# Optimization experiments

Hardware: AMD Instinct MI355X
Metric: run time of the kernel (lower is better)

## Reference

```python
import jax, jax.numpy as jnp
import numpy as np
from jax import lax

L = 50      # observation_len
P = 30      # pred_len
N = 2048    # num nearby obstacles
EMB = 64    # embed_size
NH = 128    # node_hidden_size
EH = 256    # edge_hidden_size
AD = 64     # attention_dim
CNN = 2048  # resnet50 fc.in_features


def setup_inputs() -> dict:
    key = jax.random.key(0)
    ks = jax.random.split(key, 20)
    def rn(k, shape, s=1.0):
        return jax.random.normal(k, shape, jnp.float32) * s
    w = 0.05
    return {
        "img_embedding": rn(ks[0], (1, CNN)),
        "target_obs_pos": rn(ks[1], (1, L, 2)),
        "target_obs_pos_rel": rn(ks[2], (1, L, 2)),
        "nearby_obs_pos": rn(ks[3], (1, N, L, 2)),
        "nearby_obs_pos_rel": rn(ks[4], (1, N, L, 2)),
        "nearby_obs_hist_sizes": jax.random.randint(ks[5], (1, N, 1), 0, L + 1),
        "target_obs_hist_size": L,
        "target_h0": rn(ks[6], (NH,), w),
        "target_c0": rn(ks[7], (NH,), w),
        "W_temb": rn(ks[8], (2, EMB), w), "b_temb": jnp.zeros((EMB,), jnp.float32),
        "Wih_t": rn(ks[9], (EMB, 4 * NH), w), "Whh_t": rn(ks[10], (NH, 4 * NH), w),
        "bih_t": jnp.zeros((4 * NH,), jnp.float32), "bhh_t": jnp.zeros((4 * NH,), jnp.float32),
        "W_tatt": rn(ks[11], (2, AD), w), "b_tatt": jnp.zeros((AD,), jnp.float32),
        "nearby_h0": rn(ks[12], (EH,), w),
        "nearby_c0": rn(ks[13], (EH,), w),
        "W_nemb": rn(ks[14], (2, EMB), w), "b_nemb": jnp.zeros((EMB,), jnp.float32),
        "Wih_n": rn(ks[15], (EMB, 4 * EH), w), "Whh_n": rn(ks[16], (EH, 4 * EH), w),
        "bih_n": jnp.zeros((4 * EH,), jnp.float32), "bhh_n": jnp.zeros((4 * EH,), jnp.float32),
        "W_natt": rn(ks[17], (2, AD), w), "b_natt": jnp.zeros((AD,), jnp.float32),
        "W_pred": rn(ks[18], (NH + CNN + EH, 2), w), "b_pred": jnp.zeros((2,), jnp.float32),
    }


def _lstm_cell(x, h, c, Wih, Whh, bih, bhh, H):
    # PyTorch LSTM gate order: i, f, g, o
    g = x @ Wih + h @ Whh + bih + bhh
    i = jax.nn.sigmoid(g[..., :H])
    f = jax.nn.sigmoid(g[..., H:2 * H])
    gg = jnp.tanh(g[..., 2 * H:3 * H])
    o = jax.nn.sigmoid(g[..., 3 * H:])
    c2 = f * c + i * gg
    return o * jnp.tanh(c2), c2


def _forward(img_embedding, target_obs_pos, target_obs_pos_rel, nearby_obs_pos,
             nearby_obs_pos_rel, target_h0, target_c0, W_temb, b_temb,
             Wih_t, Whh_t, bih_t, bhh_t, W_tatt, b_tatt,
             nearby_h0, nearby_c0, W_nemb, b_nemb,
             Wih_n, Whh_n, bih_n, bhh_n, W_natt, b_natt,
             W_pred, b_pred, nearby_obs_hist_sizes, target_obs_hist_size):
    nhist = nearby_obs_hist_sizes.reshape(N)
    inv_sqrt_d = 1.0 / jnp.sqrt(jnp.float32(AD))

    def attention(trel, tpos, npos, nh, nmask, Ht_prev):
        # scores scaled by curr_N / sqrt(attention_dim), softmax over masked nearby.
        # max-subtracted softmax is mathematically identical to the original exp/sum.
        currN = jnp.sum(nmask.astype(jnp.float32))
        an = (tpos - npos) @ W_natt + b_natt          # [N, AD]
        at = trel @ W_tatt + b_tatt                   # [AD]
        scores = (an @ at) * currN * inv_sqrt_d       # [N]
        w = jax.nn.softmax(jnp.where(nmask, scores, -1e30))
        return jnp.where(currN >= 1.0, w @ nh, Ht_prev)

    def obs_step(carry, x):
        th, tc, nh, nc, Ht = carry
        t, tpos, trel, npos, nrel = x
        tmask = target_obs_hist_size > (L - t)
        nmask = nhist > (L - t)
        th2, tc2 = _lstm_cell(trel @ W_temb + b_temb, th, tc, Wih_t, Whh_t, bih_t, bhh_t, NH)
        th = jnp.where(tmask, th2, th)
        tc = jnp.where(tmask, tc2, tc)
        nh2, nc2 = _lstm_cell(nrel @ W_nemb + b_nemb, nh, nc, Wih_n, Whh_n, bih_n, bhh_n, EH)
        m = nmask[:, None]
        nh = jnp.where(m, nh2, nh)
        nc = jnp.where(m, nc2, nc)
        Ht = attention(trel, tpos, npos, nh, nmask, Ht)
        return (th, tc, nh, nc, Ht), None

    np_tm = jnp.swapaxes(nearby_obs_pos[0], 0, 1)      # [L, N, 2] time-major
    nr_tm = jnp.swapaxes(nearby_obs_pos_rel[0], 0, 1)
    xs = (jnp.arange(1, L), target_obs_pos[0, 1:], target_obs_pos_rel[0, 1:],
          np_tm[1:], nr_tm[1:])
    init = (target_h0, target_c0,
            jnp.broadcast_to(nearby_h0, (N, EH)),
            jnp.broadcast_to(nearby_c0, (N, EH)),
            nearby_h0)
    (th, tc, nh, nc, Ht), _ = lax.scan(obs_step, init, xs)

    # During prediction the original reuses nearby pos/rel from the last obs step.
    npos_last = nearby_obs_pos[0, :, L - 1, :]
    nrel_last = nearby_obs_pos_rel[0, :, L - 1, :]
    xn_last = nrel_last @ W_nemb + b_nemb
    all_mask = jnp.ones((N,), bool)

    def pred_step(carry, _):
        th, tc, nh, nc, Ht, pos = carry
        pred = jnp.concatenate([th, img_embedding[0], Ht]) @ W_pred + b_pred  # [2]
        pos = pos + pred
        th, tc = _lstm_cell(pred @ W_temb + b_temb, th, tc, Wih_t, Whh_t, bih_t, bhh_t, NH)
        nh, nc = _lstm_cell(xn_last, nh, nc, Wih_n, Whh_n, bih_n, bhh_n, EH)
        Ht = attention(pred, pos, npos_last, nh, all_mask, Ht)
        return (th, tc, nh, nc, Ht, pos), pred

    carry0 = (th, tc, nh, nc, Ht, target_obs_pos[0, L - 1])
    _, preds = lax.scan(pred_step, carry0, None, length=P)
    return preds[None]                                 # [1, P, 2]


def reference(img_embedding, target_obs_pos, target_obs_pos_rel, nearby_obs_pos,
              nearby_obs_pos_rel, nearby_obs_hist_sizes, target_obs_hist_size,
              target_h0, target_c0, W_temb, b_temb, Wih_t, Whh_t, bih_t, bhh_t,
              W_tatt, b_tatt, nearby_h0, nearby_c0, W_nemb, b_nemb,
              Wih_n, Whh_n, bih_n, bhh_n, W_natt, b_natt, W_pred, b_pred):
    return _forward(img_embedding, target_obs_pos, target_obs_pos_rel, nearby_obs_pos,
                    nearby_obs_pos_rel, target_h0, target_c0, W_temb, b_temb,
                    Wih_t, Whh_t, bih_t, bhh_t, W_tatt, b_tatt,
                    nearby_h0, nearby_c0, W_nemb, b_nemb,
                    Wih_n, Whh_n, bih_n, bhh_n, W_natt, b_natt,
                    W_pred, b_pred, nearby_obs_hist_sizes, target_obs_hist_size)
```

## Files before the change

### kernel.cpp

```cpp
#include <hip/hip_runtime.h>
#include <hip/hip_bf16.h>
#include <cstdint>

#define LH   50
#define PP   30
#define NAG  2048
#define NHID 128
#define EHID 256
#define ADIM 64
#define CNND 2048

typedef __attribute__((ext_vector_type(8))) short bf16x8;
typedef __attribute__((ext_vector_type(4))) float f32x4;

enum : int {
  WS_WT  = 0,
  WS_WHT = 131072,
  WS_WFN = 163840,
  WS_BFN = 165888,
  WS_WFT = 166912,
  WS_BFT = 167936,
  WS_TH  = 168448,
  WS_TC  = 168576,
  WS_W49 = 168704,
  WS_CN  = 170752,
  WS_Z   = 170756,
  WS_END = 293636
};

__device__ __forceinline__ float sigf(float x){ return 1.0f/(1.0f + __expf(-x)); }
__device__ __forceinline__ float tanhfast(float x){
  x = fminf(15.0f, fmaxf(-15.0f, x));
  float e = __expf(2.0f*x);
  return (e - 1.0f)/(e + 1.0f);
}
__device__ __forceinline__ float bfs(short s){
  return __uint_as_float(((unsigned)(unsigned short)s) << 16);
}
__device__ __forceinline__ void gld16(const void* g, void* l){
  __builtin_amdgcn_global_load_lds(
      (const __attribute__((address_space(1))) unsigned int*)g,
      (__attribute__((address_space(3))) unsigned int*)l, 16, 0, 0);
}

__global__ void k_prep(const float* __restrict__ Whhn, const float* __restrict__ Whht,
                       const float* __restrict__ Wnemb, const float* __restrict__ bnemb,
                       const float* __restrict__ Wihn,  const float* __restrict__ bihn,
                       const float* __restrict__ bhhn,
                       const float* __restrict__ Wtemb, const float* __restrict__ btemb,
                       const float* __restrict__ Wiht,  const float* __restrict__ biht,
                       const float* __restrict__ bhht,
                       float* __restrict__ ws)
{
  const int b = blockIdx.x, tid = threadIdx.x;
  if (b < 256){
    __shared__ float t[32][33];
    __hip_bfloat16* WT = (__hip_bfloat16*)(ws + WS_WT);
    const int tx = tid & 31, ty = tid >> 5;
    const int j0 = (b & 31) << 5;
    const int e0 = (b >> 5) << 5;
    #pragma unroll
    for (int r = 0; r < 4; ++r)
      t[ty + 8*r][tx] = Whhn[(e0 + ty + 8*r)*1024 + j0 + tx];
    __syncthreads();
    const int c = e0 >> 5;
    #pragma unroll
    for (int r = 0; r < 4; ++r)
      WT[c*32768 + (j0 + ty + 8*r)*32 + tx] = __float2bfloat16(t[tx][ty + 8*r]);
  } else {
    for (int j = tid; j < 1024; j += 256){
      float a0=0.f, a1=0.f, ab=0.f;
      for (int k=0;k<64;k++){
        const float w = Wihn[k*1024 + j];
        a0 += Wnemb[k]*w; a1 += Wnemb[64+k]*w; ab += bnemb[k]*w;
      }
      ws[WS_WFN + j]        = a0;
      ws[WS_WFN + 1024 + j] = a1;
      ws[WS_BFN + j]        = ab + bihn[j] + bhhn[j];
    }
    for (int j = tid; j < 512; j += 256){
      float a0=0.f, a1=0.f, ab=0.f;
      for (int k=0;k<64;k++){
        const float w = Wiht[k*512 + j];
        a0 += Wtemb[k]*w; a1 += Wtemb[64+k]*w; ab += btemb[k]*w;
      }
      ws[WS_WFT + j]       = a0;
      ws[WS_WFT + 512 + j] = a1;
      ws[WS_BFT + j]       = ab + biht[j] + bhht[j];
    }
    __hip_bfloat16* WTt = (__hip_bfloat16*)(ws + WS_WHT);
    for (int j = tid; j < 512; j += 256)
      for (int k = 0; k < 128; ++k)
        WTt[j*128 + k] = __float2bfloat16(Whht[k*512 + j]);
  }
}

__global__ __launch_bounds__(512, 2) void k_phaseA(
    const float* __restrict__ nh0, const float* __restrict__ nc0,
    const float* __restrict__ nrel, const int* __restrict__ nhist,
    const float* __restrict__ Wpred,
    const float* __restrict__ trel, const int* __restrict__ thsp,
    const float* __restrict__ Whht, const float* __restrict__ th0,
    const float* __restrict__ tc0,
    const float* __restrict__ tpos, const float* __restrict__ npos,
    const float* __restrict__ Wtatt, const float* __restrict__ btatt,
    const float* __restrict__ Wnatt, const float* __restrict__ bnatt,
    float* __restrict__ ws)
{
  extern __shared__ char smem_raw[];
  const int b = blockIdx.x, tid = threadIdx.x;
  const int wv = tid >> 6, lane = tid & 63;
  const int lhi = lane >> 4, llo = lane & 15;

  if (b < 128){
    short* wbuf = (short*)smem_raw;
    short* Hl   = (short*)(smem_raw + 131072);
    float* relS = (float*)(smem_raw + 139520);
    float* vS   = (float*)(smem_raw + 145920);
    const int n0 = b << 4;

    for (int i = tid; i < 1600; i += 512){
      const int a = i / 100, r = i % 100;
      relS[a*100 + r] = nrel[(n0 + a)*100 + r];
    }
    if (tid < 256){
      vS[2*tid]   = Wpred[2*(NHID + CNND + tid)];
      vS[2*tid+1] = Wpred[2*(NHID + CNND + tid) + 1];
    }
    for (int i = tid; i < 4096; i += 512){
      const int a = i >> 8, e = i & 255;
      ((__hip_bfloat16*)Hl)[a*264 + e] = __float2bfloat16(nh0[e]);
    }

    float wf0[4][2], wf1[4][2], wb[4][2];
    #pragma unroll
    for (int g = 0; g < 4; ++g)
      #pragma unroll
      for (int t = 0; t < 2; ++t){
        const int j = g*256 + (wv<<5) + t*16 + llo;
        wf0[g][t] = ws[WS_WFN + j];
        wf1[g][t] = ws[WS_WFN + 1024 + j];
        wb [g][t] = ws[WS_BFN + j];
      }
    float C[4][2], ho[4][2];
    #pragma unroll
    for (int r = 0; r < 4; ++r)
      #pragma unroll
      for (int t = 0; t < 2; ++t){
        const int eo = (wv<<5) + t*16 + llo;
        C[r][t]  = nc0[eo];
        ho[r][t] = nh0[eo];
      }
    int nh4[4];
    #pragma unroll
    for (int r = 0; r < 4; ++r) nh4[r] = nhist[n0 + lhi*4 + r];

    const char* wgbase = (const char*)(ws + WS_WT);
    __syncthreads();

    {
      const char* gsrc = wgbase + wv*8192 + lane*16;
      char* ldst = (char*)wbuf + wv*8192;
      #pragma unroll
      for (int i = 0; i < 8; ++i) gld16(gsrc + i*1024, ldst + i*1024);
    }
    __syncthreads();
    int cur = 0;

    for (int st = 1; st <= 78; ++st){
      const int thr  = (st <= 49) ? (50 - st) : -1;
      const int tsel = (st <= 49) ? st : 49;

      bf16x8 af[8];
      const short* hrow = Hl + llo*264 + lhi*8;
      #pragma unroll
      for (int c = 0; c < 8; ++c) af[c] = *(const bf16x8*)(hrow + c*32);

      f32x4 acc[4][2];
      #pragma unroll
      for (int g = 0; g < 4; ++g)
        #pragma unroll
        for (int t = 0; t < 2; ++t) acc[g][t] = (f32x4){0.f,0.f,0.f,0.f};

      #pragma unroll
      for (int c = 0; c < 8; ++c){
        {
          const int nc = (c + 1) & 7;
          const char* gsrc = wgbase + nc*65536 + wv*8192 + lane*16;
          char* ldst = (char*)wbuf + (cur^1)*65536 + wv*8192;
          #pragma unroll
          for (int i = 0; i < 8; ++i) gld16(gsrc + i*1024, ldst + i*1024);
        }
        const short* bbase = wbuf + cur*32768;
        #pragma unroll
        for (int g = 0; g < 4; ++g)
          #pragma unroll
          for (int t = 0; t < 2; ++t){
            const int j = g*256 + (wv<<5) + t*16 + llo;
            const bf16x8 bf = *(const bf16x8*)(bbase + j*32 + lhi*8);
            acc[g][t] = __builtin_amdgcn_mfma_f32_16x16x32_bf16(af[c], bf, acc[g][t], 0,0,0);
          }
        __syncthreads();
        cur ^= 1;
      }

      #pragma unroll
      for (int r = 0; r < 4; ++r){
        const float r0 = relS[(lhi*4 + r)*100 + 2*tsel];
        const float r1 = relS[(lhi*4 + r)*100 + 2*tsel + 1];
        const bool mk = nh4[r] > thr;
        #pragma unroll
        for (int t = 0; t < 2; ++t){
          const float gi = acc[0][t][r] + r0*wf0[0][t] + r1*wf1[0][t] + wb[0][t];
          const float gf = acc[1][t][r] + r0*wf0[1][t] + r1*wf1[1][t] + wb[1][t];
          const float gg = acc[2][t][r] + r0*wf0[2][t] + r1*wf1[2][t] + wb[2][t];
          const float go = acc[3][t][r] + r0*wf0[3][t] + r1*wf1[3][t] + wb[3][t];
          const float c2 = sigf(gf)*C[r][t] + sigf(gi)*tanhfast(gg);
          const float h2 = sigf(go)*tanhfast(c2);
          if (mk){ C[r][t] = c2; ho[r][t] = h2; }
        }
      }
      #pragma unroll
      for (int r = 0; r < 4; ++r)
        #pragma unroll
        for (int t = 0; t < 2; ++t)
          ((__hip_bfloat16*)Hl)[(lhi*4 + r)*264 + (wv<<5) + t*16 + llo] =
              __float2bfloat16(ho[r][t]);
      __syncthreads();

      if (st >= 49){
        const int s = st - 49;
        const int a = wv*2 + (lane >> 5);
        const int sub = lane & 31;
        float z0 = 0.f, z1 = 0.f;
        const short* hp = Hl + a*264 + sub*8;
        #pragma unroll
        for (int i = 0; i < 8; ++i){
          const float h = bfs(hp[i]);
          z0 += h*vS[2*(sub*8 + i)];
          z1 += h*vS[2*(sub*8 + i) + 1];
        }
        #pragma unroll
        for (int o = 16; o > 0; o >>= 1){
          z0 += __shfl_down(z0, o, 32);
          z1 += __shfl_down(z1, o, 32);
        }
        if (sub == 0){
          ws[WS_Z + (s*NAG + n0 + a)*2]     = z0;
          ws[WS_Z + (s*NAG + n0 + a)*2 + 1] = z1;
        }
      }
    }
  }
  else if (b == 128){
    float* hT = (float*)smem_raw;
    float* cT = hT + 128;
    float* gT = cT + 128;
    if (tid < 128){ hT[tid] = th0[tid]; cT[tid] = tc0[tid]; }
    __syncthreads();
    const int ths = thsp[0];
    for (int t = 1; t < 50; ++t){
      const float x0 = trel[2*t], x1 = trel[2*t+1];
      float acc = x0*ws[WS_WFT + tid] + x1*ws[WS_WFT + 512 + tid] + ws[WS_BFT + tid];
      for (int k = 0; k < 128; ++k) acc += hT[k]*Whht[k*512 + tid];
      gT[tid] = acc;
      __syncthreads();
      if (tid < 128 && ths > 50 - t){
        const float ig = sigf(gT[tid]),          fg = sigf(gT[128 + tid]);
        const float gg = tanhfast(gT[256 + tid]), og = sigf(gT[384 + tid]);
        const float c2 = fg*cT[tid] + ig*gg;
        cT[tid] = c2; hT[tid] = og*tanhfast(c2);
      }
      __syncthreads();
    }
    if (tid < 128){ ws[WS_TH + tid] = hT[tid]; ws[WS_TC + tid] = cT[tid]; }
  }
  else {
    float* at  = (float*)smem_raw;
    float* red = at + 64;
    float* uv  = red + 512;
    const int t = LH - 1;
    const float tr0 = trel[2*t], tr1 = trel[2*t+1];
    const float tp0 = tpos[2*t], tp1 = tpos[2*t+1];
    if (tid < ADIM) at[tid] = tr0*Wtatt[tid] + tr1*Wtatt[ADIM+tid] + btatt[tid];
    int cnt = 0;
    #pragma unroll
    for (int i = 0; i < 4; ++i) cnt += (nhist[tid + 512*i] > (LH - t)) ? 1 : 0;
    red[tid] = (float)cnt;
    __syncthreads();
    if (tid == 0){
      float u0=0.f,u1=0.f,v=0.f;
      for (int k=0;k<ADIM;k++){ u0 += Wnatt[k]*at[k]; u1 += Wnatt[ADIM+k]*at[k]; v += bnatt[k]*at[k]; }
      uv[0]=u0; uv[1]=u1; uv[2]=v;
    }
    for (int s = 256; s > 0; s >>= 1){ if (tid < s) red[tid] += red[tid+s]; __syncthreads(); }
    const float currN = red[0];
    __syncthreads();
    const float u0 = uv[0], u1 = uv[1], v = uv[2];
    const float scale = currN * 0.125f;
    float sc[4]; float smax = -3.0e38f;
    #pragma unroll
    for (int i = 0; i < 4; ++i){
      const int n = tid + 512*i;
      const float p0 = npos[n*100 + 2*t], p1 = npos[n*100 + 2*t + 1];
      float s = scale * ((tp0-p0)*u0 + (tp1-p1)*u1 + v);
      s = (nhist[n] > (LH - t)) ? s : -1.0e30f;
      sc[i] = s; smax = fmaxf(smax, s);
    }
    red[tid] = smax; __syncthreads();
    for (int s = 256; s > 0; s >>= 1){ if (tid<s) red[tid] = fmaxf(red[tid], red[tid+s]); __syncthreads(); }
    smax = red[0]; __syncthreads();
    float ssum = 0.f;
    #pragma unroll
    for (int i = 0; i < 4; ++i){ sc[i] = __expf(sc[i]-smax); ssum += sc[i]; }
    red[tid] = ssum; __syncthreads();
    for (int s = 256; s > 0; s >>= 1){ if (tid<s) red[tid] += red[tid+s]; __syncthreads(); }
    const float inv = 1.0f / red[0];
    #pragma unroll
    for (int i = 0; i < 4; ++i) ws[WS_W49 + tid + 512*i] = sc[i]*inv;
    if (tid == 0) ws[WS_CN] = currN;
  }
}

template<int K>
__device__ __forceinline__ void bredN(const float* v, volatile float* scratch,
                                      volatile float* outv, int tid){
  const int lane = tid & 63, wv = tid >> 6;
  #pragma unroll
  for (int k = 0; k < K; ++k){
    float x = v[k];
    #pragma unroll
    for (int o = 32; o > 0; o >>= 1) x += __shfl_down(x, o, 64);
    if (lane == 0) scratch[k*8 + wv] = x;
  }
  __syncthreads();
  if (tid == 0){
    #pragma unroll
    for (int k = 0; k < K; ++k){
      float s = 0.f;
      for (int i = 0; i < 8; ++i) s += scratch[k*8 + i];
      outv[k] = s;
    }
  }
  __syncthreads();
}

__device__ __forceinline__ float bredMax1(float x, volatile float* scratch,
                                          volatile float* outv, int tid){
  const int lane = tid & 63, wv = tid >> 6;
  #pragma unroll
  for (int o = 32; o > 0; o >>= 1) x = fmaxf(x, __shfl_down(x, o, 64));
  if (lane == 0) scratch[wv] = x;
  __syncthreads();
  if (tid == 0){
    float s = -3.0e38f;
    for (int i = 0; i < 8; ++i) s = fmaxf(s, scratch[i]);
    outv[0] = s;
  }
  __syncthreads();
  return outv[0];
}

__global__ __launch_bounds__(512, 1) void k_phaseB(
    const float* __restrict__ img, const float* __restrict__ tpos,
    const float* __restrict__ npos, const float* __restrict__ nh0,
    const float* __restrict__ Wpred, const float* __restrict__ bpred,
    const float* __restrict__ Wtatt, const float* __restrict__ btatt,
    const float* __restrict__ Wnatt, const float* __restrict__ bnatt,
    float* __restrict__ ws, float* __restrict__ out)
{
  __shared__ float p0s[NAG], p1s[NAG];
  __shared__ float th[128], tc[128], gl[512], at[64];
// ... 110 lines not shown
      float uu1 = Wnatt[ADIM + lane]*at[lane];
      float vv  = bnatt[lane]*at[lane];
      #pragma unroll
      for (int o = 32; o > 0; o >>= 1){
        uu0 += __shfl_down(uu0, o, 64);
        uu1 += __shfl_down(uu1, o, 64);
        vv  += __shfl_down(vv,  o, 64);
      }
      if (lane == 0){
        bc[4] = uu0; bc[5] = uu1;
        bc[6] = pos0*uu0 + pos1*uu1 + vv;
      }
    }
    __syncthreads();
    u0 = bc[4]; u1 = bc[5]; A = bc[6];
  }
}

extern "C" void kernel_launch(void* const* d_in, const int* in_sizes, int n_in,
                              void* d_out, int out_size, void* d_ws, size_t ws_size,
                              hipStream_t stream) {
  const float* img   = (const float*)d_in[0];
  const float* tpos  = (const float*)d_in[1];
  const float* trel  = (const float*)d_in[2];
  const float* npos  = (const float*)d_in[3];
  const float* nrel  = (const float*)d_in[4];
  const int*   nhist = (const int*)d_in[5];
  const int*   ths   = (const int*)d_in[6];
  const float* th0   = (const float*)d_in[7];
  const float* tc0   = (const float*)d_in[8];
  const float* Wtemb = (const float*)d_in[9];
  const float* btemb = (const float*)d_in[10];
  const float* Wiht  = (const float*)d_in[11];
  const float* Whht  = (const float*)d_in[12];
  const float* biht  = (const float*)d_in[13];
  const float* bhht  = (const float*)d_in[14];
  const float* Wtatt = (const float*)d_in[15];
  const float* btatt = (const float*)d_in[16];
  const float* nh0   = (const float*)d_in[17];
  const float* nc0   = (const float*)d_in[18];
  const float* Wnemb = (const float*)d_in[19];
  const float* bnemb = (const float*)d_in[20];
  const float* Wihn  = (const float*)d_in[21];
  const float* Whhn  = (const float*)d_in[22];
  const float* bihn  = (const float*)d_in[23];
  const float* bhhn  = (const float*)d_in[24];
  const float* Wnatt = (const float*)d_in[25];
  const float* bnatt = (const float*)d_in[26];
  const float* Wpred = (const float*)d_in[27];
  const float* bpred = (const float*)d_in[28];
  float* ws  = (float*)d_ws;
  float* out = (float*)d_out;

  k_prep<<<257, 256, 0, stream>>>(Whhn, Whht, Wnemb, bnemb, Wihn, bihn, bhhn,
                                  Wtemb, btemb, Wiht, biht, bhht, ws);
  k_phaseA<<<130, 512, 147968, stream>>>(nh0, nc0, nrel, nhist, Wpred,
                                         trel, ths, Whht, th0, tc0,
                                         tpos, npos, Wtatt, btatt, Wnatt, bnatt, ws);
  k_phaseB<<<1, 512, 0, stream>>>(img, tpos, npos, nh0, Wpred, bpred,
                                  Wtatt, btatt, Wnatt, bnatt, ws, out);
}
```

Measured before the change: 890.3 us.

## Keep half of recurrent LSTM weights in registers, stream rest with swizzled LDS

The first half of the K dimension of the nearby-agent recurrent weight matrix now lives in per-wave registers for the whole recurrence. Only the second half is streamed from global memory through a double-buffered LDS ring, using a new XOR-swizzled layout built in the prep kernel. Manual waitcnt/s_barrier fences replace __syncthreads, and the H row stride is padded to reduce bank conflicts. This halves per-step weight traffic into LDS at the cost of much higher register pressure and more fragile hand-written synchronisation.

```diff
diff --git a/kernel.cpp b/kernel.cpp
--- a/kernel.cpp
+++ b/kernel.cpp
@@ -15,6 +15,7 @@
 
 enum : int {
   WS_WT  = 0,
+  WS_WZ  = 65536,
   WS_WHT = 131072,
   WS_WFN = 163840,
   WS_BFN = 165888,
@@ -28,6 +29,8 @@
   WS_END = 293636
 };
 
+#define HLROW 280
+
 __device__ __forceinline__ float sigf(float x){ return 1.0f/(1.0f + __expf(-x)); }
 __device__ __forceinline__ float tanhfast(float x){
   x = fminf(15.0f, fmaxf(-15.0f, x));
@@ -53,7 +56,7 @@
                        float* __restrict__ ws)
 {
   const int b = blockIdx.x, tid = threadIdx.x;
-  if (b < 256){
+  if (b < 128){
     __shared__ float t[32][33];
     __hip_bfloat16* WT = (__hip_bfloat16*)(ws + WS_WT);
     const int tx = tid & 31, ty = tid >> 5;
@@ -67,6 +70,19 @@
     #pragma unroll
     for (int r = 0; r < 4; ++r)
       WT[c*32768 + (j0 + ty + 8*r)*32 + tx] = __float2bfloat16(t[tx][ty + 8*r]);
+  } else if (b < 192){
+    __hip_bfloat16* WZ = (__hip_bfloat16*)(ws + WS_WZ);
+    const int bb = b - 128;
+    const int c  = bb >> 4;
+    const int r0 = (bb & 15) << 5;
+    const int r  = r0 + (tid >> 3);
+    const int p  = tid & 7;
+    const int ls = p ^ (r & 7);
+    const int j  = ((ls >> 2) << 9) + r;
+    const int kb = (4 + c)*32 + (ls & 3)*8;
+    #pragma unroll
+    for (int i = 0; i < 8; ++i)
+      WZ[((c*512 + r)*8 + p)*8 + i] = __float2bfloat16(Whhn[(kb + i)*1024 + j]);
   } else {
     for (int j = tid; j < 1024; j += 256){
       float a0=0.f, a1=0.f, ab=0.f;
@@ -115,10 +131,33 @@
   if (b < 128){
     short* wbuf = (short*)smem_raw;
     short* Hl   = (short*)(smem_raw + 131072);
-    float* relS = (float*)(smem_raw + 139520);
-    float* vS   = (float*)(smem_raw + 145920);
+    float* relS = (float*)(smem_raw + 131072 + 16*HLROW*2);
+    float* vS   = relS + 1600;
     const int n0 = b << 4;
 
+    {
+      const char* wz = (const char*)(ws + WS_WZ);
+      #pragma unroll
+      for (int bufc = 0; bufc < 2; ++bufc){
+        const char* gsrc = wz + bufc*65536 + wv*8192 + lane*16;
+        char* ldst = smem_raw + bufc*65536 + wv*8192;
+        #pragma unroll
+        for (int i = 0; i < 8; ++i) gld16(gsrc + i*1024, ldst + i*1024);
+      }
+    }
+    bf16x8 wreg[4][2][4];
+    {
+      const short* wt = (const short*)(ws + WS_WT);
+      #pragma unroll
+      for (int g = 0; g < 4; ++g)
+        #pragma unroll
+        for (int t = 0; t < 2; ++t){
+          const int j = g*256 + (wv<<5) + t*16 + llo;
+          #pragma unroll
+          for (int ks = 0; ks < 4; ++ks)
+            wreg[g][t][ks] = *(const bf16x8*)(wt + ks*32768 + j*32 + lhi*8);
+        }
+    }
     for (int i = tid; i < 1600; i += 512){
       const int a = i / 100, r = i % 100;
       relS[a*100 + r] = nrel[(n0 + a)*100 + r];
@@ -129,9 +168,8 @@
     }
     for (int i = tid; i < 4096; i += 512){
       const int a = i >> 8, e = i & 255;
-      ((__hip_bfloat16*)Hl)[a*264 + e] = __float2bfloat16(nh0[e]);
-    }
-
+      ((__hip_bfloat16*)Hl)[a*HLROW + e] = __float2bfloat16(nh0[e]);
+    }
     float wf0[4][2], wf1[4][2], wb[4][2];
     #pragma unroll
     for (int g = 0; g < 4; ++g)
@@ -155,27 +193,12 @@
     #pragma unroll
     for (int r = 0; r < 4; ++r) nh4[r] = nhist[n0 + lhi*4 + r];
 
-    const char* wgbase = (const char*)(ws + WS_WT);
-    __syncthreads();
-
-    {
-      const char* gsrc = wgbase + wv*8192 + lane*16;
-      char* ldst = (char*)wbuf + wv*8192;
-      #pragma unroll
-      for (int i = 0; i < 8; ++i) gld16(gsrc + i*1024, ldst + i*1024);
-    }
-    __syncthreads();
-    int cur = 0;
+    __syncthreads();
 
     for (int st = 1; st <= 78; ++st){
       const int thr  = (st <= 49) ? (50 - st) : -1;
       const int tsel = (st <= 49) ? st : 49;
 
-      bf16x8 af[8];
-      const short* hrow = Hl + llo*264 + lhi*8;
-      #pragma unroll
-      for (int c = 0; c < 8; ++c) af[c] = *(const bf16x8*)(hrow + c*32);
-
       f32x4 acc[4][2];
       #pragma unroll
       for (int g = 0; g < 4; ++g)
@@ -183,25 +206,44 @@
         for (int t = 0; t < 2; ++t) acc[g][t] = (f32x4){0.f,0.f,0.f,0.f};
 
       #pragma unroll
-      for (int c = 0; c < 8; ++c){
-        {
-          const int nc = (c + 1) & 7;
-          const char* gsrc = wgbase + nc*65536 + wv*8192 + lane*16;
-          char* ldst = (char*)wbuf + (cur^1)*65536 + wv*8192;
+      for (int ks = 0; ks < 4; ++ks){
+        const bf16x8 afr = *(const bf16x8*)(Hl + llo*HLROW + ks*32 + lhi*8);
+        #pragma unroll
+        for (int g = 0; g < 4; ++g)
           #pragma unroll
-          for (int i = 0; i < 8; ++i) gld16(gsrc + i*1024, ldst + i*1024);
-        }
-        const short* bbase = wbuf + cur*32768;
+          for (int t = 0; t < 2; ++t)
+            acc[g][t] = __builtin_amdgcn_mfma_f32_16x16x32_bf16(afr, wreg[g][t][ks], acc[g][t], 0,0,0);
+      }
+
+      #pragma unroll
+      for (int i = 0; i < 4; ++i){
+        const bf16x8 afs = *(const bf16x8*)(Hl + llo*HLROW + (4+i)*32 + lhi*8);
+        asm volatile("s_waitcnt vmcnt(8)" ::: "memory");
+        __builtin_amdgcn_sched_barrier(0);
+        __builtin_amdgcn_s_barrier();
+        __builtin_amdgcn_sched_barrier(0);
+        const short* bb = wbuf + (i & 1)*32768;
         #pragma unroll
         for (int g = 0; g < 4; ++g)
           #pragma unroll
           for (int t = 0; t < 2; ++t){
-            const int j = g*256 + (wv<<5) + t*16 + llo;
-            const bf16x8 bf = *(const bf16x8*)(bbase + j*32 + lhi*8);
-            acc[g][t] = __builtin_amdgcn_mfma_f32_16x16x32_bf16(af[c], bf, acc[g][t], 0,0,0);
+            const int r  = ((g & 1) << 8) + (wv << 5) + t*16 + llo;
+            const int ls = ((g >> 1) << 2) + lhi;
+            const int p  = ls ^ (r & 7);
+            const bf16x8 bfv = *(const bf16x8*)(bb + r*64 + p*8);
+            acc[g][t] = __builtin_amdgcn_mfma_f32_16x16x32_bf16(afs, bfv, acc[g][t], 0,0,0);
           }
-        __syncthreads();
-        cur ^= 1;
+        asm volatile("s_waitcnt lgkmcnt(0)" ::: "memory");
+        __builtin_amdgcn_sched_barrier(0);
+        __builtin_amdgcn_s_barrier();
+        __builtin_amdgcn_sched_barrier(0);
+        {
+          const int nc = (i + 2) & 3;
+          const char* gsrc = (const char*)(ws + WS_WZ) + nc*65536 + wv*8192 + lane*16;
+          char* ldst = smem_raw + (i & 1)*65536 + wv*8192;
+          #pragma unroll
+          for (int q = 0; q < 8; ++q) gld16(gsrc + q*1024, ldst + q*1024);
+        }
       }
 
       #pragma unroll
@@ -224,16 +266,19 @@
       for (int r = 0; r < 4; ++r)
         #pragma unroll
         for (int t = 0; t < 2; ++t)
-          ((__hip_bfloat16*)Hl)[(lhi*4 + r)*264 + (wv<<5) + t*16 + llo] =
+          ((__hip_bfloat16*)Hl)[(lhi*4 + r)*HLROW + (wv<<5) + t*16 + llo] =
               __float2bfloat16(ho[r][t]);
-      __syncthreads();
+      asm volatile("s_waitcnt lgkmcnt(0)" ::: "memory");
+      __builtin_amdgcn_sched_barrier(0);
+      __builtin_amdgcn_s_barrier();
+      __builtin_amdgcn_sched_barrier(0);
 
       if (st >= 49){
         const int s = st - 49;
         const int a = wv*2 + (lane >> 5);
         const int sub = lane & 31;
         float z0 = 0.f, z1 = 0.f;
-        const short* hp = Hl + a*264 + sub*8;
+        const short* hp = Hl + a*HLROW + sub*8;
         #pragma unroll
         for (int i = 0; i < 8; ++i){
           const float h = bfs(hp[i]);
@@ -534,11 +579,13 @@
   float* ws  = (float*)d_ws;
   float* out = (float*)d_out;
 
-  k_prep<<<257, 256, 0, stream>>>(Whhn, Whht, Wnemb, bnemb, Wihn, bihn, bhhn,
+  const int ldsA = 131072 + 16*HLROW*2 + 1600*4 + 512*4;
+
+  k_prep<<<193, 256, 0, stream>>>(Whhn, Whht, Wnemb, bnemb, Wihn, bihn, bhhn,
                                   Wtemb, btemb, Wiht, biht, bhht, ws);
-  k_phaseA<<<130, 512, 147968, stream>>>(nh0, nc0, nrel, nhist, Wpred,
-                                         trel, ths, Whht, th0, tc0,
-                                         tpos, npos, Wtatt, btatt, Wnatt, bnatt, ws);
+  k_phaseA<<<130, 512, ldsA, stream>>>(nh0, nc0, nrel, nhist, Wpred,
+                                       trel, ths, Whht, th0, tc0,
+                                       tpos, npos, Wtatt, btatt, Wnatt, bnatt, ws);
   k_phaseB<<<1, 512, 0, stream>>>(img, tpos, npos, nh0, Wpred, bpred,
                                   Wtatt, btatt, Wnatt, bnatt, ws, out);
 }
```

Result: slower. 937.6 us (+5.3%).

## Keep recurrent LSTM weights resident in registers and LDS instead of restreaming

Applied to the files above, without the earlier changes.

The nearby-agent LSTM kernel previously streamed the full bf16 Whh matrix from global memory into double-buffered LDS on every one of the 78 steps, with a barrier per chunk. Now each block loads the weights once: 6 of 8 K-chunks live in VGPRs per wave and the other 2 sit in LDS. The hidden state is double-buffered in LDS so only one barrier per step is needed. This removes repeated global weight traffic and the per-chunk syncs, at the cost of very high register pressure, with launch bounds relaxed to 1 block per CU.

```diff
diff --git a/kernel.cpp b/kernel.cpp
--- a/kernel.cpp
+++ b/kernel.cpp
@@ -28,6 +28,8 @@
   WS_END = 293636
 };
 
+#define HLH 4224
+
 __device__ __forceinline__ float sigf(float x){ return 1.0f/(1.0f + __expf(-x)); }
 __device__ __forceinline__ float tanhfast(float x){
   x = fminf(15.0f, fmaxf(-15.0f, x));
@@ -36,11 +38,6 @@
 }
 __device__ __forceinline__ float bfs(short s){
   return __uint_as_float(((unsigned)(unsigned short)s) << 16);
-}
-__device__ __forceinline__ void gld16(const void* g, void* l){
-  __builtin_amdgcn_global_load_lds(
-      (const __attribute__((address_space(1))) unsigned int*)g,
-      (__attribute__((address_space(3))) unsigned int*)l, 16, 0, 0);
 }
 
 __global__ void k_prep(const float* __restrict__ Whhn, const float* __restrict__ Whht,
@@ -95,7 +92,7 @@
   }
 }
 
-__global__ __launch_bounds__(512, 2) void k_phaseA(
+__global__ __launch_bounds__(512, 1) void k_phaseA(
     const float* __restrict__ nh0, const float* __restrict__ nc0,
     const float* __restrict__ nrel, const int* __restrict__ nhist,
     const float* __restrict__ Wpred,
@@ -107,22 +104,37 @@
     const float* __restrict__ Wnatt, const float* __restrict__ bnatt,
     float* __restrict__ ws)
 {
-  extern __shared__ char smem_raw[];
+  extern __shared__ char smem[];
   const int b = blockIdx.x, tid = threadIdx.x;
   const int wv = tid >> 6, lane = tid & 63;
   const int lhi = lane >> 4, llo = lane & 15;
 
   if (b < 128){
-    short* wbuf = (short*)smem_raw;
-    short* Hl   = (short*)(smem_raw + 131072);
-    float* relS = (float*)(smem_raw + 139520);
-    float* vS   = (float*)(smem_raw + 145920);
+    short* wlds = (short*)smem;
+    short* Hl   = (short*)(smem + 131072);
+    float* wfS  = (float*)(smem + 147968);
+    float* vS   = (float*)(smem + 160256);
     const int n0 = b << 4;
-
-    for (int i = tid; i < 1600; i += 512){
-      const int a = i / 100, r = i % 100;
-      relS[a*100 + r] = nrel[(n0 + a)*100 + r];
-    }
+    const int jcol = (wv << 5) + llo;
+    const short* wt = (const short*)(ws + WS_WT);
+
+    bf16x8 wreg[4][2][4];
+    bf16x8 s67[4][2][2];
+    #pragma unroll
+    for (int g = 0; g < 4; ++g)
+      #pragma unroll
+      for (int t = 0; t < 2; ++t){
+        const int j = g*256 + jcol + t*16;
+        #pragma unroll
+        for (int ks = 0; ks < 4; ++ks)
+          wreg[g][t][ks] = *(const bf16x8*)(wt + ks*32768 + j*32 + lhi*8);
+        #pragma unroll
+        for (int i = 0; i < 2; ++i)
+          s67[g][t][i] = *(const bf16x8*)(wt + (6+i)*32768 + j*32 + lhi*8);
+      }
+    for (int i = tid; i < 8192; i += 512)
+      *(uint4*)(wlds + i*8) = *(const uint4*)(wt + 4*32768 + i*8);
+    for (int i = tid; i < 3072; i += 512) wfS[i] = ws[WS_WFN + i];
     if (tid < 256){
       vS[2*tid]   = Wpred[2*(NHID + CNND + tid)];
       vS[2*tid+1] = Wpred[2*(NHID + CNND + tid) + 1];
@@ -131,50 +143,20 @@
       const int a = i >> 8, e = i & 255;
       ((__hip_bfloat16*)Hl)[a*264 + e] = __float2bfloat16(nh0[e]);
     }
-
-    float wf0[4][2], wf1[4][2], wb[4][2];
-    #pragma unroll
-    for (int g = 0; g < 4; ++g)
-      #pragma unroll
-      for (int t = 0; t < 2; ++t){
-        const int j = g*256 + (wv<<5) + t*16 + llo;
-        wf0[g][t] = ws[WS_WFN + j];
-        wf1[g][t] = ws[WS_WFN + 1024 + j];
-        wb [g][t] = ws[WS_BFN + j];
-      }
-    float C[4][2], ho[4][2];
+    float C[4][2];
     #pragma unroll
     for (int r = 0; r < 4; ++r)
       #pragma unroll
-      for (int t = 0; t < 2; ++t){
-        const int eo = (wv<<5) + t*16 + llo;
-        C[r][t]  = nc0[eo];
-        ho[r][t] = nh0[eo];
-      }
-    int nh4[4];
-    #pragma unroll
-    for (int r = 0; r < 4; ++r) nh4[r] = nhist[n0 + lhi*4 + r];
-
-    const char* wgbase = (const char*)(ws + WS_WT);
-    __syncthreads();
-
-    {
-      const char* gsrc = wgbase + wv*8192 + lane*16;
-      char* ldst = (char*)wbuf + wv*8192;
-      #pragma unroll
-      for (int i = 0; i < 8; ++i) gld16(gsrc + i*1024, ldst + i*1024);
-    }
-    __syncthreads();
+      for (int t = 0; t < 2; ++t)
+        C[r][t] = nc0[jcol + t*16];
+
+    __syncthreads();
+
     int cur = 0;
-
     for (int st = 1; st <= 78; ++st){
       const int thr  = (st <= 49) ? (50 - st) : -1;
       const int tsel = (st <= 49) ? st : 49;
-
-      bf16x8 af[8];
-      const short* hrow = Hl + llo*264 + lhi*8;
-      #pragma unroll
-      for (int c = 0; c < 8; ++c) af[c] = *(const bf16x8*)(hrow + c*32);
+      const short* hc = Hl + cur*HLH + llo*264 + lhi*8;
 
       f32x4 acc[4][2];
       #pragma unroll
@@ -183,62 +165,87 @@
         for (int t = 0; t < 2; ++t) acc[g][t] = (f32x4){0.f,0.f,0.f,0.f};
 
       #pragma unroll
-      for (int c = 0; c < 8; ++c){
-        {
-          const int nc = (c + 1) & 7;
-          const char* gsrc = wgbase + nc*65536 + wv*8192 + lane*16;
-          char* ldst = (char*)wbuf + (cur^1)*65536 + wv*8192;
+      for (int ks = 0; ks < 4; ++ks){
+        const bf16x8 af = *(const bf16x8*)(hc + ks*32);
+        #pragma unroll
+        for (int g = 0; g < 4; ++g)
           #pragma unroll
-          for (int i = 0; i < 8; ++i) gld16(gsrc + i*1024, ldst + i*1024);
-        }
-        const short* bbase = wbuf + cur*32768;
+          for (int t = 0; t < 2; ++t)
+            acc[g][t] = __builtin_amdgcn_mfma_f32_16x16x32_bf16(af, wreg[g][t][ks], acc[g][t], 0,0,0);
+      }
+      #pragma unroll
+      for (int i = 0; i < 2; ++i){
+        const bf16x8 af = *(const bf16x8*)(hc + (4+i)*32);
         #pragma unroll
         for (int g = 0; g < 4; ++g)
           #pragma unroll
           for (int t = 0; t < 2; ++t){
-            const int j = g*256 + (wv<<5) + t*16 + llo;
-            const bf16x8 bf = *(const bf16x8*)(bbase + j*32 + lhi*8);
-            acc[g][t] = __builtin_amdgcn_mfma_f32_16x16x32_bf16(af[c], bf, acc[g][t], 0,0,0);
+            const bf16x8 bw = *(const bf16x8*)(wlds + i*32768 + (g*256 + jcol + t*16)*32 + lhi*8);
+            acc[g][t] = __builtin_amdgcn_mfma_f32_16x16x32_bf16(af, bw, acc[g][t], 0,0,0);
           }
-        __syncthreads();
-        cur ^= 1;
-      }
-
-      #pragma unroll
-      for (int r = 0; r < 4; ++r){
-        const float r0 = relS[(lhi*4 + r)*100 + 2*tsel];
-        const float r1 = relS[(lhi*4 + r)*100 + 2*tsel + 1];
-        const bool mk = nh4[r] > thr;
+      }
+      #pragma unroll
+      for (int i = 0; i < 2; ++i){
+        const bf16x8 af = *(const bf16x8*)(hc + (6+i)*32);
+        #pragma unroll
+        for (int g = 0; g < 4; ++g)
+          #pragma unroll
+          for (int t = 0; t < 2; ++t)
+            acc[g][t] = __builtin_amdgcn_mfma_f32_16x16x32_bf16(af, s67[g][t][i], acc[g][t], 0,0,0);
+      }
+
+      {
+        float2 rr[4]; bool mk[4];
+        #pragma unroll
+        for (int r = 0; r < 4; ++r){
+          const int ag = n0 + lhi*4 + r;
+          rr[r] = *(const float2*)(nrel + ag*100 + 2*tsel);
+          mk[r] = nhist[ag] > thr;
+        }
+        volatile float* wfv = wfS;
+        short* hn = Hl + (cur^1)*HLH;
+        const short* ho = Hl + cur*HLH;
         #pragma unroll
         for (int t = 0; t < 2; ++t){
-          const float gi = acc[0][t][r] + r0*wf0[0][t] + r1*wf1[0][t] + wb[0][t];
-          const float gf = acc[1][t][r] + r0*wf0[1][t] + r1*wf1[1][t] + wb[1][t];
-          const float gg = acc[2][t][r] + r0*wf0[2][t] + r1*wf1[2][t] + wb[2][t];
-          const float go = acc[3][t][r] + r0*wf0[3][t] + r1*wf1[3][t] + wb[3][t];
-          const float c2 = sigf(gf)*C[r][t] + sigf(gi)*tanhfast(gg);
-          const float h2 = sigf(go)*tanhfast(c2);
-          if (mk){ C[r][t] = c2; ho[r][t] = h2; }
+          const int j0 = jcol + t*16;
+          float wfa[4], wfb[4], wbb[4];
+          #pragma unroll
+          for (int g = 0; g < 4; ++g){
+            wfa[g] = wfv[g*256 + j0];
+            wfb[g] = wfv[1024 + g*256 + j0];
+            wbb[g] = wfv[2048 + g*256 + j0];
+          }
+          #pragma unroll
+          for (int r = 0; r < 4; ++r){
+            const int ag = lhi*4 + r;
+            const float gi = acc[0][t][r] + rr[r].x*wfa[0] + rr[r].y*wfb[0] + wbb[0];
+            const float gf = acc[1][t][r] + rr[r].x*wfa[1] + rr[r].y*wfb[1] + wbb[1];
+            const float gg = acc[2][t][r] + rr[r].x*wfa[2] + rr[r].y*wfb[2] + wbb[2];
+            const float go = acc[3][t][r] + rr[r].x*wfa[3] + rr[r].y*wfb[3] + wbb[3];
+            const float c2 = sigf(gf)*C[r][t] + sigf(gi)*tanhfast(gg);
+            const float h2 = sigf(go)*tanhfast(c2);
+            const short hold = ho[ag*264 + j0];
+            short hnew; { __hip_bfloat16 hb = __float2bfloat16(h2); hnew = *(short*)&hb; }
+            if (mk[r]) C[r][t] = c2;
+            hn[ag*264 + j0] = mk[r] ? hnew : hold;
+          }
         }
       }
-      #pragma unroll
-      for (int r = 0; r < 4; ++r)
-        #pragma unroll
-        for (int t = 0; t < 2; ++t)
-          ((__hip_bfloat16*)Hl)[(lhi*4 + r)*264 + (wv<<5) + t*16 + llo] =
-              __float2bfloat16(ho[r][t]);
       __syncthreads();
+      cur ^= 1;
 
       if (st >= 49){
         const int s = st - 49;
         const int a = wv*2 + (lane >> 5);
         const int sub = lane & 31;
+        const short* hp = Hl + cur*HLH + a*264 + sub*8;
+        volatile float* vv = vS;
         float z0 = 0.f, z1 = 0.f;
-        const short* hp = Hl + a*264 + sub*8;
         #pragma unroll
         for (int i = 0; i < 8; ++i){
           const float h = bfs(hp[i]);
-          z0 += h*vS[2*(sub*8 + i)];
-          z1 += h*vS[2*(sub*8 + i) + 1];
+          z0 += h*vv[2*(sub*8 + i)];
+          z1 += h*vv[2*(sub*8 + i) + 1];
         }
         #pragma unroll
         for (int o = 16; o > 0; o >>= 1){
@@ -253,7 +260,7 @@
     }
   }
   else if (b == 128){
-    float* hT = (float*)smem_raw;
+    float* hT = (float*)smem;
     float* cT = hT + 128;
     float* gT = cT + 128;
     if (tid < 128){ hT[tid] = th0[tid]; cT[tid] = tc0[tid]; }
@@ -276,7 +283,7 @@
     if (tid < 128){ ws[WS_TH + tid] = hT[tid]; ws[WS_TC + tid] = cT[tid]; }
   }
   else {
-    float* at  = (float*)smem_raw;
+    float* at  = (float*)smem;
     float* red = at + 64;
     float* uv  = red + 512;
     const int t = LH - 1;
@@ -534,11 +541,13 @@
   float* ws  = (float*)d_ws;
   float* out = (float*)d_out;
 
+  const int ldsA = 131072 + 16896 + 3072*4 + 512*4;
+
   k_prep<<<257, 256, 0, stream>>>(Whhn, Whht, Wnemb, bnemb, Wihn, bihn, bhhn,
                                   Wtemb, btemb, Wiht, biht, bhht, ws);
-  k_phaseA<<<130, 512, 147968, stream>>>(nh0, nc0, nrel, nhist, Wpred,
-                                         trel, ths, Whht, th0, tc0,
-                                         tpos, npos, Wtatt, btatt, Wnatt, bnatt, ws);
+  k_phaseA<<<130, 512, ldsA, stream>>>(nh0, nc0, nrel, nhist, Wpred,
+                                       trel, ths, Whht, th0, tc0,
+                                       tpos, npos, Wtatt, btatt, Wnatt, bnatt, ws);
   k_phaseB<<<1, 512, 0, stream>>>(img, tpos, npos, nh0, Wpred, bpred,
                                   Wtatt, btatt, Wnatt, bnatt, ws, out);
 }
```

Result: slower. 968.9 us, median of 2 (+8.8%).

## Restructure nearby-LSTM recurrence: register-resident weight chunk, 256-thread blocks, double-buffered H

Applied to the files above, without the earlier changes.

Phase A now runs 256 threads per block. Each wave owns 64 gate columns, and the first K-chunk of the recurrent weights stays in registers. The remaining seven chunks stream through a two-deep LDS pipeline with explicit waitcnt and barrier scheduling, and the weight layout is re-tiled to match. The hidden state is double-buffered in LDS, which removes one barrier per step. Per-step output projections are collected in LDS and written out once at the end. The aim is to cut global weight-streaming and synchronization overhead in the 78-step serial loop, at the cost of higher register pressure and fewer waves per block.

```diff
diff --git a/kernel.cpp b/kernel.cpp
--- a/kernel.cpp
+++ b/kernel.cpp
@@ -58,15 +58,15 @@
     __hip_bfloat16* WT = (__hip_bfloat16*)(ws + WS_WT);
     const int tx = tid & 31, ty = tid >> 5;
     const int j0 = (b & 31) << 5;
-    const int e0 = (b >> 5) << 5;
+    const int c  = b >> 5;
+    const int e0 = c << 5;
     #pragma unroll
     for (int r = 0; r < 4; ++r)
       t[ty + 8*r][tx] = Whhn[(e0 + ty + 8*r)*1024 + j0 + tx];
     __syncthreads();
-    const int c = e0 >> 5;
     #pragma unroll
     for (int r = 0; r < 4; ++r)
-      WT[c*32768 + (j0 + ty + 8*r)*32 + tx] = __float2bfloat16(t[tx][ty + 8*r]);
+      WT[c*32768 + r*8192 + (j0 + tx)*8 + ty] = __float2bfloat16(t[ty + 8*r][tx]);
   } else {
     for (int j = tid; j < 1024; j += 256){
       float a0=0.f, a1=0.f, ab=0.f;
@@ -95,7 +95,14 @@
   }
 }
 
-__global__ __launch_bounds__(512, 2) void k_phaseA(
+#define STAGE(cc, bb_) do { \
+  const char* gsrc_ = wgl + (cc)*65536 + wv*16384 + lane*16; \
+  char* ldst_ = (char*)wbuf + (bb_)*65536 + wv*16384; \
+  _Pragma("unroll") \
+  for (int q_ = 0; q_ < 16; ++q_) gld16(gsrc_ + q_*1024, ldst_ + q_*1024); \
+} while(0)
+
+__global__ __launch_bounds__(256, 1) void k_phaseA(
     const float* __restrict__ nh0, const float* __restrict__ nc0,
     const float* __restrict__ nrel, const int* __restrict__ nhist,
     const float* __restrict__ Wpred,
@@ -107,19 +114,47 @@
     const float* __restrict__ Wnatt, const float* __restrict__ bnatt,
     float* __restrict__ ws)
 {
-  extern __shared__ char smem_raw[];
+  extern __shared__ char smem[];
   const int b = blockIdx.x, tid = threadIdx.x;
   const int wv = tid >> 6, lane = tid & 63;
   const int lhi = lane >> 4, llo = lane & 15;
 
   if (b < 128){
-    short* wbuf = (short*)smem_raw;
-    short* Hl   = (short*)(smem_raw + 131072);
-    float* relS = (float*)(smem_raw + 139520);
-    float* vS   = (float*)(smem_raw + 145920);
+    short* wbuf = (short*)smem;
+    short* Hl   = (short*)(smem + 131072);
+    float* relS = (float*)(smem + 147968);
+    float* vS   = (float*)(smem + 154368);
+    float* zS   = (float*)(smem + 156416);
     const int n0 = b << 4;
-
-    for (int i = tid; i < 1600; i += 512){
+    const short* wt = (const short*)(ws + WS_WT);
+    const char*  wgl = (const char*)wt;
+
+    bf16x8 wreg[4][4];
+    float wfa[4][4], wfb[4][4], wbb[4][4];
+    #pragma unroll
+    for (int g = 0; g < 4; ++g)
+      #pragma unroll
+      for (int t = 0; t < 4; ++t){
+        const int j = g*256 + (wv<<6) + t*16 + llo;
+        wreg[g][t] = *(const bf16x8*)(wt + lhi*8192 + j*8);
+        wfa[g][t] = ws[WS_WFN + j];
+        wfb[g][t] = ws[WS_WFN + 1024 + j];
+        wbb[g][t] = ws[WS_BFN + j];
+      }
+    float C[4][4];
+    #pragma unroll
+    for (int r = 0; r < 4; ++r)
+      #pragma unroll
+      for (int t = 0; t < 4; ++t)
+        C[r][t] = nc0[(wv<<6) + t*16 + llo];
+    int nh4[4];
+    #pragma unroll
+    for (int r = 0; r < 4; ++r) nh4[r] = nhist[n0 + lhi*4 + r];
+
+    STAGE(1, 0);
+    STAGE(2, 1);
+
+    for (int i = tid; i < 1600; i += 256){
       const int a = i / 100, r = i % 100;
       relS[a*100 + r] = nrel[(n0 + a)*100 + r];
     }
@@ -127,133 +162,117 @@
       vS[2*tid]   = Wpred[2*(NHID + CNND + tid)];
       vS[2*tid+1] = Wpred[2*(NHID + CNND + tid) + 1];
     }
-    for (int i = tid; i < 4096; i += 512){
+    for (int i = tid; i < 4096; i += 256){
       const int a = i >> 8, e = i & 255;
       ((__hip_bfloat16*)Hl)[a*264 + e] = __float2bfloat16(nh0[e]);
     }
-
-    float wf0[4][2], wf1[4][2], wb[4][2];
-    #pragma unroll
-    for (int g = 0; g < 4; ++g)
-      #pragma unroll
-      for (int t = 0; t < 2; ++t){
-        const int j = g*256 + (wv<<5) + t*16 + llo;
-        wf0[g][t] = ws[WS_WFN + j];
-        wf1[g][t] = ws[WS_WFN + 1024 + j];
-        wb [g][t] = ws[WS_BFN + j];
-      }
-    float C[4][2], ho[4][2];
-    #pragma unroll
-    for (int r = 0; r < 4; ++r)
-      #pragma unroll
-      for (int t = 0; t < 2; ++t){
-        const int eo = (wv<<5) + t*16 + llo;
-        C[r][t]  = nc0[eo];
-        ho[r][t] = nh0[eo];
-      }
-    int nh4[4];
-    #pragma unroll
-    for (int r = 0; r < 4; ++r) nh4[r] = nhist[n0 + lhi*4 + r];
-
-    const char* wgbase = (const char*)(ws + WS_WT);
-    __syncthreads();
-
-    {
-      const char* gsrc = wgbase + wv*8192 + lane*16;
-      char* ldst = (char*)wbuf + wv*8192;
-      #pragma unroll
-      for (int i = 0; i < 8; ++i) gld16(gsrc + i*1024, ldst + i*1024);
-    }
-    __syncthreads();
-    int cur = 0;
-
+    __syncthreads();
+
+    int cur = 0, ccons = 1, cnext = 3, pb = 0;
     for (int st = 1; st <= 78; ++st){
       const int thr  = (st <= 49) ? (50 - st) : -1;
       const int tsel = (st <= 49) ? st : 49;
-
-      bf16x8 af[8];
-      const short* hrow = Hl + llo*264 + lhi*8;
-      #pragma unroll
-      for (int c = 0; c < 8; ++c) af[c] = *(const bf16x8*)(hrow + c*32);
-
-      f32x4 acc[4][2];
+      const short* hc = Hl + cur*4224 + llo*264 + lhi*8;
+
+      f32x4 acc[4][4];
       #pragma unroll
       for (int g = 0; g < 4; ++g)
         #pragma unroll
-        for (int t = 0; t < 2; ++t) acc[g][t] = (f32x4){0.f,0.f,0.f,0.f};
-
-      #pragma unroll
-      for (int c = 0; c < 8; ++c){
-        {
-          const int nc = (c + 1) & 7;
-          const char* gsrc = wgbase + nc*65536 + wv*8192 + lane*16;
-          char* ldst = (char*)wbuf + (cur^1)*65536 + wv*8192;
-          #pragma unroll
-          for (int i = 0; i < 8; ++i) gld16(gsrc + i*1024, ldst + i*1024);
-        }
-        const short* bbase = wbuf + cur*32768;
+        for (int t = 0; t < 4; ++t) acc[g][t] = (f32x4){0.f,0.f,0.f,0.f};
+
+      {
+        const bf16x8 af0 = *(const bf16x8*)(hc);
         #pragma unroll
         for (int g = 0; g < 4; ++g)
           #pragma unroll
-          for (int t = 0; t < 2; ++t){
-            const int j = g*256 + (wv<<5) + t*16 + llo;
-            const bf16x8 bf = *(const bf16x8*)(bbase + j*32 + lhi*8);
-            acc[g][t] = __builtin_amdgcn_mfma_f32_16x16x32_bf16(af[c], bf, acc[g][t], 0,0,0);
+          for (int t = 0; t < 4; ++t)
+            acc[g][t] = __builtin_amdgcn_mfma_f32_16x16x32_bf16(af0, wreg[g][t], acc[g][t], 0,0,0);
+      }
+      for (int p = 0; p < 7; ++p){
+        asm volatile("s_waitcnt vmcnt(16)" ::: "memory");
+        __builtin_amdgcn_sched_barrier(0);
+        __builtin_amdgcn_s_barrier();
+        __builtin_amdgcn_sched_barrier(0);
+        const short* bb = wbuf + pb*32768;
+        const bf16x8 afs = *(const bf16x8*)(hc + ccons*32);
+        #pragma unroll
+        for (int g = 0; g < 4; ++g)
+          #pragma unroll
+          for (int t = 0; t < 4; ++t){
+            const int j = g*256 + (wv<<6) + t*16 + llo;
+            const bf16x8 bw = *(const bf16x8*)(bb + lhi*8192 + j*8);
+            acc[g][t] = __builtin_amdgcn_mfma_f32_16x16x32_bf16(afs, bw, acc[g][t], 0,0,0);
           }
-        __syncthreads();
-        cur ^= 1;
-      }
-
-      #pragma unroll
-      for (int r = 0; r < 4; ++r){
-        const float r0 = relS[(lhi*4 + r)*100 + 2*tsel];
-        const float r1 = relS[(lhi*4 + r)*100 + 2*tsel + 1];
-        const bool mk = nh4[r] > thr;
-        #pragma unroll
-        for (int t = 0; t < 2; ++t){
-          const float gi = acc[0][t][r] + r0*wf0[0][t] + r1*wf1[0][t] + wb[0][t];
-          const float gf = acc[1][t][r] + r0*wf0[1][t] + r1*wf1[1][t] + wb[1][t];
-          const float gg = acc[2][t][r] + r0*wf0[2][t] + r1*wf1[2][t] + wb[2][t];
-          const float go = acc[3][t][r] + r0*wf0[3][t] + r1*wf1[3][t] + wb[3][t];
-          const float c2 = sigf(gf)*C[r][t] + sigf(gi)*tanhfast(gg);
-          const float h2 = sigf(go)*tanhfast(c2);
-          if (mk){ C[r][t] = c2; ho[r][t] = h2; }
+        asm volatile("s_waitcnt lgkmcnt(0)" ::: "memory");
+        __builtin_amdgcn_sched_barrier(0);
+        __builtin_amdgcn_s_barrier();
+        __builtin_amdgcn_sched_barrier(0);
+        STAGE(cnext, pb);
+        ccons = (ccons == 7) ? 1 : ccons + 1;
+        cnext = (cnext == 7) ? 1 : cnext + 1;
+        pb ^= 1;
+      }
+
+      {
+        short* hn = Hl + (cur^1)*4224;
+        const short* ho = Hl + cur*4224;
+        float2 rr[4];
+        #pragma unroll
+        for (int r = 0; r < 4; ++r)
+          rr[r] = *(const float2*)(relS + (lhi*4 + r)*100 + 2*tsel);
+        #pragma unroll
+        for (int t = 0; t < 4; ++t){
+          const int e = (wv<<6) + t*16 + llo;
+          #pragma unroll
+          for (int r = 0; r < 4; ++r){
+            const int ag = lhi*4 + r;
+            const float gi = acc[0][t][r] + rr[r].x*wfa[0][t] + rr[r].y*wfb[0][t] + wbb[0][t];
+            const float gf = acc[1][t][r] + rr[r].x*wfa[1][t] + rr[r].y*wfb[1][t] + wbb[1][t];
+            const float gg = acc[2][t][r] + rr[r].x*wfa[2][t] + rr[r].y*wfb[2][t] + wbb[2][t];
+            const float go = acc[3][t][r] + rr[r].x*wfa[3][t] + rr[r].y*wfb[3][t] + wbb[3][t];
+            const float c2 = sigf(gf)*C[r][t] + sigf(gi)*tanhfast(gg);
+            const float h2 = sigf(go)*tanhfast(c2);
+            const bool mk = nh4[r] > thr;
+            if (mk) C[r][t] = c2;
+            const short hold = ho[ag*264 + e];
+            short hnew; { __hip_bfloat16 hb = __float2bfloat16(h2); hnew = *(short*)&hb; }
+            hn[ag*264 + e] = mk ? hnew : hold;
+          }
         }
       }
-      #pragma unroll
-      for (int r = 0; r < 4; ++r)
-        #pragma unroll
-        for (int t = 0; t < 2; ++t)
-          ((__hip_bfloat16*)Hl)[(lhi*4 + r)*264 + (wv<<5) + t*16 + llo] =
-              __float2bfloat16(ho[r][t]);
       __syncthreads();
+      cur ^= 1;
 
       if (st >= 49){
         const int s = st - 49;
-        const int a = wv*2 + (lane >> 5);
-        const int sub = lane & 31;
+        const int a = tid >> 4, sub = tid & 15;
+        const short* hp = Hl + cur*4224 + a*264 + sub*16;
         float z0 = 0.f, z1 = 0.f;
-        const short* hp = Hl + a*264 + sub*8;
-        #pragma unroll
-        for (int i = 0; i < 8; ++i){
+        #pragma unroll
+        for (int i = 0; i < 16; ++i){
           const float h = bfs(hp[i]);
-          z0 += h*vS[2*(sub*8 + i)];
-          z1 += h*vS[2*(sub*8 + i) + 1];
+          z0 += h*vS[2*(sub*16 + i)];
+          z1 += h*vS[2*(sub*16 + i) + 1];
         }
         #pragma unroll
-        for (int o = 16; o > 0; o >>= 1){
-          z0 += __shfl_down(z0, o, 32);
-          z1 += __shfl_down(z1, o, 32);
+        for (int o = 8; o > 0; o >>= 1){
+          z0 += __shfl_down(z0, o, 16);
+          z1 += __shfl_down(z1, o, 16);
         }
         if (sub == 0){
-          ws[WS_Z + (s*NAG + n0 + a)*2]     = z0;
-          ws[WS_Z + (s*NAG + n0 + a)*2 + 1] = z1;
+          zS[s*32 + a*2]     = z0;
+          zS[s*32 + a*2 + 1] = z1;
         }
       }
     }
+    __syncthreads();
+    for (int i = tid; i < 960; i += 256){
+      const int s = i >> 5, rem = i & 31;
+      ws[WS_Z + (s*NAG + n0 + (rem >> 1))*2 + (rem & 1)] = zS[i];
+    }
   }
   else if (b == 128){
-    float* hT = (float*)smem_raw;
+    float* hT = (float*)smem;
     float* cT = hT + 128;
     float* gT = cT + 128;
     if (tid < 128){ hT[tid] = th0[tid]; cT[tid] = tc0[tid]; }
@@ -261,9 +280,13 @@
     const int ths = thsp[0];
     for (int t = 1; t < 50; ++t){
       const float x0 = trel[2*t], x1 = trel[2*t+1];
-      float acc = x0*ws[WS_WFT + tid] + x1*ws[WS_WFT + 512 + tid] + ws[WS_BFT + tid];
-      for (int k = 0; k < 128; ++k) acc += hT[k]*Whht[k*512 + tid];
-      gT[tid] = acc;
+      #pragma unroll
+      for (int q = 0; q < 2; ++q){
+        const int j = tid + q*256;
+        float acc = x0*ws[WS_WFT + j] + x1*ws[WS_WFT + 512 + j] + ws[WS_BFT + j];
+        for (int k = 0; k < 128; ++k) acc += hT[k]*Whht[k*512 + j];
+        gT[j] = acc;
+      }
       __syncthreads();
       if (tid < 128 && ths > 50 - t){
         const float ig = sigf(gT[tid]),          fg = sigf(gT[128 + tid]);
@@ -276,16 +299,16 @@
     if (tid < 128){ ws[WS_TH + tid] = hT[tid]; ws[WS_TC + tid] = cT[tid]; }
   }
   else {
-    float* at  = (float*)smem_raw;
+    float* at  = (float*)smem;
     float* red = at + 64;
-    float* uv  = red + 512;
+    float* uv  = red + 256;
     const int t = LH - 1;
     const float tr0 = trel[2*t], tr1 = trel[2*t+1];
     const float tp0 = tpos[2*t], tp1 = tpos[2*t+1];
     if (tid < ADIM) at[tid] = tr0*Wtatt[tid] + tr1*Wtatt[ADIM+tid] + btatt[tid];
     int cnt = 0;
     #pragma unroll
-    for (int i = 0; i < 4; ++i) cnt += (nhist[tid + 512*i] > (LH - t)) ? 1 : 0;
+    for (int i = 0; i < 8; ++i) cnt += (nhist[tid + 256*i] > (LH - t)) ? 1 : 0;
     red[tid] = (float)cnt;
     __syncthreads();
     if (tid == 0){
@@ -293,31 +316,31 @@
       for (int k=0;k<ADIM;k++){ u0 += Wnatt[k]*at[k]; u1 += Wnatt[ADIM+k]*at[k]; v += bnatt[k]*at[k]; }
       uv[0]=u0; uv[1]=u1; uv[2]=v;
     }
-    for (int s = 256; s > 0; s >>= 1){ if (tid < s) red[tid] += red[tid+s]; __syncthreads(); }
+    for (int s = 128; s > 0; s >>= 1){ if (tid < s) red[tid] += red[tid+s]; __syncthreads(); }
     const float currN = red[0];
     __syncthreads();
     const float u0 = uv[0], u1 = uv[1], v = uv[2];
     const float scale = currN * 0.125f;
-    float sc[4]; float smax = -3.0e38f;
-    #pragma unroll
-    for (int i = 0; i < 4; ++i){
-      const int n = tid + 512*i;
+    float sc[8]; float smax = -3.0e38f;
+    #pragma unroll
+    for (int i = 0; i < 8; ++i){
+      const int n = tid + 256*i;
       const float p0 = npos[n*100 + 2*t], p1 = npos[n*100 + 2*t + 1];
       float s = scale * ((tp0-p0)*u0 + (tp1-p1)*u1 + v);
       s = (nhist[n] > (LH - t)) ? s : -1.0e30f;
       sc[i] = s; smax = fmaxf(smax, s);
     }
     red[tid] = smax; __syncthreads();
-    for (int s = 256; s > 0; s >>= 1){ if (tid<s) red[tid] = fmaxf(red[tid], red[tid+s]); __syncthreads(); }
+    for (int s = 128; s > 0; s >>= 1){ if (tid<s) red[tid] = fmaxf(red[tid], red[tid+s]); __syncthreads(); }
     smax = red[0]; __syncthreads();
     float ssum = 0.f;
     #pragma unroll
-    for (int i = 0; i < 4; ++i){ sc[i] = __expf(sc[i]-smax); ssum += sc[i]; }
+    for (int i = 0; i < 8; ++i){ sc[i] = __expf(sc[i]-smax); ssum += sc[i]; }
     red[tid] = ssum; __syncthreads();
-    for (int s = 256; s > 0; s >>= 1){ if (tid<s) red[tid] += red[tid+s]; __syncthreads(); }
+    for (int s = 128; s > 0; s >>= 1){ if (tid<s) red[tid] += red[tid+s]; __syncthreads(); }
     const float inv = 1.0f / red[0];
     #pragma unroll
-    for (int i = 0; i < 4; ++i) ws[WS_W49 + tid + 512*i] = sc[i]*inv;
+    for (int i = 0; i < 8; ++i) ws[WS_W49 + tid + 256*i] = sc[i]*inv;
     if (tid == 0) ws[WS_CN] = currN;
   }
 }
@@ -534,11 +557,13 @@
   float* ws  = (float*)d_ws;
   float* out = (float*)d_out;
 
+  const int ldsA = 160256;
+
   k_prep<<<257, 256, 0, stream>>>(Whhn, Whht, Wnemb, bnemb, Wihn, bihn, bhhn,
                                   Wtemb, btemb, Wiht, biht, bhht, ws);
-  k_phaseA<<<130, 512, 147968, stream>>>(nh0, nc0, nrel, nhist, Wpred,
-                                         trel, ths, Whht, th0, tc0,
-                                         tpos, npos, Wtatt, btatt, Wnatt, bnatt, ws);
+  k_phaseA<<<130, 256, ldsA, stream>>>(nh0, nc0, nrel, nhist, Wpred,
+                                       trel, ths, Whht, th0, tc0,
+                                       tpos, npos, Wtatt, btatt, Wnatt, bnatt, ws);
   k_phaseB<<<1, 512, 0, stream>>>(img, tpos, npos, nh0, Wpred, bpred,
                                   Wtatt, btatt, Wnatt, bnatt, ws, out);
 }
```

Result: slower. 1.058 ms (+18.8%).
